# Kernel optimization log

Hardware: AMD Instinct MI355X
Metric: run time of the kernel (lower is better)

## Reference

```python
import jax, jax.numpy as jnp
import numpy as np

HEADS = 8
HEAD_DIM = 32
FOLD = 2
PROP = 2


def l2norm(t):
    n = jnp.linalg.norm(t, axis=-1, keepdims=True)
    return t / jnp.maximum(n, 1e-12)


def conv1x1(x, w, b):
    # x: [B,C,W,H], w: [O,C]
    return jnp.einsum('bchw,oc->bohw', x, w) + b[None, :, None, None]


def avg_pool_to(x, ow, oh):
    b, c, w, h = x.shape
    return x.reshape(b, c, ow, w // ow, oh, h // oh).mean(axis=(3, 5))


def max_pool_to(x, ow, oh):
    b, c, w, h = x.shape
    return x.reshape(b, c, ow, w // ow, oh, h // oh).max(axis=(3, 5))


def centers_offset(x, w1, b1, w2, b2):
    # Mlp_new_offset: avg-pool to (H//4,W//4), channel MLP, max-pool to (2,2)
    b, c, H, W = x.shape
    y = avg_pool_to(x, H // 4, W // 4).transpose(0, 2, 3, 1)  # [b,h4,w4,c]
    y = jax.nn.gelu(y @ w1.T + b1, approximate=False) @ w2.T + b2
    return max_pool_to(y.transpose(0, 3, 1, 2), PROP, PROP)


def fold(t, f):
    b, c, W, H = t.shape
    w, h = W // f, H // f
    return t.reshape(b, c, f, w, f, h).transpose(0, 2, 4, 1, 3, 5).reshape(b * f * f, c, w, h)


def unfold(t, f):
    bf, c, w, h = t.shape
    b = bf // (f * f)
    return t.reshape(b, f, f, c, w, h).transpose(0, 3, 1, 4, 2, 5).reshape(b, c, f * w, f * h)


def setup_inputs() -> dict:
    key = jax.random.key(0)
    ks = jax.random.split(key, 12)
    B, DIM, W, H = 16, 256, 64, 64
    HD = HEADS * HEAD_DIM
    hid = int(HEAD_DIM * 1.66)  # 53
    r = lambda k, s: 0.02 * jax.random.normal(k, s, dtype=jnp.float32)
    return dict(
        x=jax.random.normal(ks[0], (B, DIM, W, H), dtype=jnp.float32),
        gap_scaler=1e-5 * jnp.ones((1, DIM, 1, 1), jnp.float32),
        w_fc1=r(ks[1], (HD, DIM)), b_fc1=r(ks[2], (HD,)),
        w_fcv=r(ks[3], (HD, DIM)), b_fcv=r(ks[4], (HD,)),
        w_fc2=r(ks[5], (DIM, HD)), b_fc2=r(ks[6], (DIM,)),
        sim_alpha=jnp.ones((1,), jnp.float32),
        sim_beta=jnp.zeros((1,), jnp.float32),
        off_w1=r(ks[7], (hid, HEAD_DIM)), off_b1=r(ks[8], (hid,)),
        off_w2=r(ks[9], (HEAD_DIM, hid)), off_b2=r(ks[10], (HEAD_DIM,)),
    )


def reference(x, gap_scaler, w_fc1, b_fc1, w_fcv, b_fcv, w_fc2, b_fc2,
              sim_alpha, sim_beta, off_w1, off_b1, off_w2, off_b2):
    B = x.shape[0]
    x = x + gap_scaler * x.mean(axis=(2, 3), keepdims=True)
    value = conv1x1(x, w_fcv, b_fcv)
    x = conv1x1(x, w_fc1, b_fc1)
    _, _, W, H = x.shape
    Bh = B * HEADS
    x = x.reshape(Bh, HEAD_DIM, W, H)
    value = value.reshape(Bh, HEAD_DIM, W, H)
    x = fold(x, FOLD)
    value = fold(value, FOLD)
    b, c, w, h = x.shape
    N, M = w * h, PROP * PROP
    centers = avg_pool_to(x, PROP, PROP) + centers_offset(x, off_w1, off_b1, off_w2, off_b2)
    value_centers = (avg_pool_to(value, PROP, PROP)
                     + centers_offset(value, off_w1, off_b1, off_w2, off_b2)
                     ).reshape(b, c, M).transpose(0, 2, 1)  # [b,M,c]
    cn = l2norm(centers.reshape(b, c, M).transpose(0, 2, 1))  # [b,M,c]
    xn = l2norm(x.reshape(b, c, N).transpose(0, 2, 1))        # [b,N,c]
    sim = jax.nn.sigmoid(sim_beta + sim_alpha * jnp.einsum('bmc,bnc->bmn', cn, xn))
    # top-1 assignment per token (scatter-built mask in torch)
    idx = jnp.argmax(sim, axis=1)  # [b,N]
    mask = (jnp.arange(M)[None, :, None] == idx[:, None, :]).astype(sim.dtype)
    sim = sim * mask
    value2 = value.reshape(b, c, N).transpose(0, 2, 1)  # [b,N,c]
    # combine: masked weighted sum of tokens into clusters (fused einsum,
    # same math as (value2[:,None]*sim[...,None]).sum(2))
    out = (jnp.einsum('bmn,bnc->bmc', sim, value2) + value_centers) / (mask.sum(-1, keepdims=True) + 1.0)
    # dispatch: broadcast cluster features back to tokens
    out = jnp.einsum('bmc,bmn->bnc', out, sim)
    out = out.transpose(0, 2, 1).reshape(b, c, w, h)
    out = unfold(out, FOLD).reshape(B, HEADS * HEAD_DIM, W, H)
    return conv1x1(out, w_fc2, b_fc2)
```

## Files before the change

### kernel.cpp

```cpp
#include <hip/hip_runtime.h>
#include <hip/hip_bf16.h>
#include <math.h>

#define HID 53

typedef __bf16 bf16x8 __attribute__((ext_vector_type(8)));
typedef float f32x4 __attribute__((ext_vector_type(4)));

__device__ __forceinline__ unsigned f2u(float f) { return __builtin_bit_cast(unsigned, f); }
__device__ __forceinline__ float u2f(unsigned u) { return __builtin_bit_cast(float, u); }
__device__ __forceinline__ bf16x8 ld8(const ushort* p) {
    return __builtin_bit_cast(bf16x8, *(const uint4*)p);
}
__device__ __forceinline__ unsigned rnb(float f) {
    unsigned u = f2u(f);
    return (u + 0x7FFFu + ((u >> 16) & 1u)) >> 16;
}
__device__ __forceinline__ void split3rn(float f, unsigned& h, unsigned& m, unsigned& l) {
    h = rnb(f);
    float r1 = f - u2f(h << 16);
    m = rnb(r1);
    float r2 = r1 - u2f(m << 16);
    l = rnb(r2);
}

__device__ __forceinline__ ushort f2bf(float f) {
    return __builtin_bit_cast(ushort, (__bf16)f);
}
__device__ __forceinline__ float bfbits2f(ushort h) { return u2f((unsigned)h << 16); }
__device__ __forceinline__ void split3c(float f, ushort& h, ushort& m, ushort& l) {
    h = f2bf(f);
    float r1 = f - bfbits2f(h);
    m = f2bf(r1);
    float r2 = r1 - bfbits2f(m);
    l = f2bf(r2);
}

__global__ __launch_bounds__(256) void mean_kernel(
    const float* __restrict__ x, const float* __restrict__ gap,
    float* __restrict__ gmu)
{
    const int bc = blockIdx.x;
    const float* p = x + (size_t)bc * 4096;
    float s = 0.f;
    for (int i = threadIdx.x * 4; i < 4096; i += 256 * 4) {
        float4 v = *(const float4*)(p + i);
        s += v.x + v.y + v.z + v.w;
    }
    s += __shfl_xor(s, 1);
    s += __shfl_xor(s, 2);
    s += __shfl_xor(s, 4);
    s += __shfl_xor(s, 8);
    s += __shfl_xor(s, 16);
    s += __shfl_xor(s, 32);
    __shared__ float ls[4];
    if ((threadIdx.x & 63) == 0) ls[threadIdx.x >> 6] = s;
    __syncthreads();
    if (threadIdx.x == 0) {
        float t = ls[0] + ls[1] + ls[2] + ls[3];
        gmu[bc] = gap[bc & 255] * (t * (1.f / 4096.f));
    }
}

__global__ __launch_bounds__(256, 2) void gemm_xq6_kernel(
    const float* __restrict__ X, const float* __restrict__ gmu,
    const float* __restrict__ W,
    const float* __restrict__ bias_g,
    float* __restrict__ dst)
{
    __shared__ __align__(16) ushort Ahi[128 * 40];
    __shared__ __align__(16) ushort Amd[128 * 40];
    __shared__ __align__(16) ushort Alo[128 * 40];
    __shared__ __align__(16) ushort Bhi[128 * 40];
    __shared__ __align__(16) ushort Bmd[128 * 40];
    __shared__ __align__(16) ushort Blo[128 * 40];

    const int tid  = threadIdx.x;
    const int Nblk = blockIdx.x, Mblk = blockIdx.y, b = blockIdx.z;
    const int lane = tid & 63, wav = tid >> 6;
    const int wm = wav >> 1, wn = wav & 1;
    const int lr = lane & 15, q = lane >> 4;

    f32x4 accM[4][4], accS[4][4];
#pragma unroll
    for (int i = 0; i < 4; ++i)
#pragma unroll
        for (int j = 0; j < 4; ++j) {
            accM[i][j] = (f32x4){0.f, 0.f, 0.f, 0.f};
            accS[i][j] = (f32x4){0.f, 0.f, 0.f, 0.f};
        }

    const bool isB = (tid < 128);
    float4 regs[8];
    float gval0 = 0.f, gval1 = 0.f;
    const float* srcB = X;
    const float* wrow = W;
    int kp = 0, q8 = 0, arow = 0;
    if (isB) {
        kp = tid >> 3; q8 = tid & 7;
        srcB = X + ((size_t)b << 20) + (size_t)(2 * kp) * 4096 + Nblk * 128 + q8 * 4;
    } else {
        arow = tid - 128;
        int o = Mblk * 128 + arow;
        wrow = W + (size_t)o * 256;
    }

    auto LOADR = [&](int ks) {
        const int k0 = ks * 32;
        if (isB) {
            const float* p = srcB + (size_t)k0 * 4096;
#pragma unroll
            for (int i = 0; i < 4; ++i) {
                regs[i]     = *(const float4*)(p + i * 32);
                regs[i + 4] = *(const float4*)(p + 4096 + i * 32);
            }
            gval0 = gmu[b * 256 + k0 + 2 * kp];
            gval1 = gmu[b * 256 + k0 + 2 * kp + 1];
        } else {
            const float* p = wrow + k0;
#pragma unroll
            for (int i = 0; i < 8; ++i) regs[i] = *(const float4*)(p + i * 4);
        }
    };

    auto WRITE = [&]() {
        if (isB) {
#pragma unroll
            for (int i = 0; i < 4; ++i) {
                float4 r0 = regs[i], r1 = regs[i + 4];
                r0.x += gval0; r0.y += gval0; r0.z += gval0; r0.w += gval0;
                r1.x += gval1; r1.y += gval1; r1.z += gval1; r1.w += gval1;
                const float* p0 = &r0.x;
                const float* p1 = &r1.x;
#pragma unroll
                for (int e = 0; e < 4; ++e) {
                    ushort h0, m0, l0, h1, m1, l1;
                    split3c(p0[e], h0, m0, l0);
                    split3c(p1[e], h1, m1, l1);
                    int n = q8 * 4 + i * 32 + e;
                    ((unsigned*)Bhi)[n * 20 + kp] = (unsigned)h0 | ((unsigned)h1 << 16);
                    ((unsigned*)Bmd)[n * 20 + kp] = (unsigned)m0 | ((unsigned)m1 << 16);
                    ((unsigned*)Blo)[n * 20 + kp] = (unsigned)l0 | ((unsigned)l1 << 16);
                }
            }
        } else {
#pragma unroll
            for (int i = 0; i < 8; ++i) {
                float4 r = regs[i];
                ushort h0, m0, l0, h1, m1, l1, h2, m2, l2, h3, m3, l3;
                split3c(r.x, h0, m0, l0);
                split3c(r.y, h1, m1, l1);
                split3c(r.z, h2, m2, l2);
                split3c(r.w, h3, m3, l3);
                uint2 h = {(unsigned)h0 | ((unsigned)h1 << 16),
                           (unsigned)h2 | ((unsigned)h3 << 16)};
                uint2 m = {(unsigned)m0 | ((unsigned)m1 << 16),
                           (unsigned)m2 | ((unsigned)m3 << 16)};
                uint2 l = {(unsigned)l0 | ((unsigned)l1 << 16),
                           (unsigned)l2 | ((unsigned)l3 << 16)};
                *(uint2*)&Ahi[arow * 40 + i * 4] = h;
                *(uint2*)&Amd[arow * 40 + i * 4] = m;
                *(uint2*)&Alo[arow * 40 + i * 4] = l;
            }
        }
    };

    LOADR(0);
    for (int ks = 0; ks < 8; ++ks) {
        WRITE();
        __syncthreads();
        if (ks < 7) LOADR(ks + 1);

        bf16x8 ah[4], ad[4];
#pragma unroll
        for (int mt = 0; mt < 4; ++mt) {
            int row = wm * 64 + mt * 16 + lr;
            ah[mt] = ld8(&Ahi[row * 40 + q * 8]);
            ad[mt] = ld8(&Amd[row * 40 + q * 8]);
        }
#pragma unroll
        for (int nt = 0; nt < 4; ++nt) {
            int row = wn * 64 + nt * 16 + lr;
            bf16x8 bh = ld8(&Bhi[row * 40 + q * 8]);
            bf16x8 bd = ld8(&Bmd[row * 40 + q * 8]);
            bf16x8 bl = ld8(&Blo[row * 40 + q * 8]);
#pragma unroll
            for (int mt = 0; mt < 4; ++mt) {
                accS[mt][nt] = __builtin_amdgcn_mfma_f32_16x16x32_bf16(ah[mt], bd, accS[mt][nt], 0, 0, 0);
                accS[mt][nt] = __builtin_amdgcn_mfma_f32_16x16x32_bf16(ad[mt], bh, accS[mt][nt], 0, 0, 0);
                accS[mt][nt] = __builtin_amdgcn_mfma_f32_16x16x32_bf16(ad[mt], bd, accS[mt][nt], 0, 0, 0);
                accS[mt][nt] = __builtin_amdgcn_mfma_f32_16x16x32_bf16(ah[mt], bl, accS[mt][nt], 0, 0, 0);
                accM[mt][nt] = __builtin_amdgcn_mfma_f32_16x16x32_bf16(ah[mt], bh, accM[mt][nt], 0, 0, 0);
            }
        }
        bf16x8 al[4];
#pragma unroll
        for (int mt = 0; mt < 4; ++mt) {
            int row = wm * 64 + mt * 16 + lr;
            al[mt] = ld8(&Alo[row * 40 + q * 8]);
        }
#pragma unroll
        for (int nt = 0; nt < 4; ++nt) {
            int row = wn * 64 + nt * 16 + lr;
            bf16x8 bh2 = ld8(&Bhi[row * 40 + q * 8]);
#pragma unroll
            for (int mt = 0; mt < 4; ++mt)
                accS[mt][nt] = __builtin_amdgcn_mfma_f32_16x16x32_bf16(al[mt], bh2, accS[mt][nt], 0, 0, 0);
        }
        __syncthreads();
    }

    const size_t bbase = (size_t)b << 20;
    const int tb = Nblk * 128 + wn * 64 + lr;
    int offN[4];
#pragma unroll
    for (int nt = 0; nt < 4; ++nt) {
        int t = tb + nt * 16;
        offN[nt] = ((t >> 11) & 1) * 65536 + ((t >> 5) & 1) * 32768
                 + ((t >> 6) & 31) * 32 + (t & 31);
    }
#pragma unroll
    for (int mt = 0; mt < 4; ++mt) {
#pragma unroll
        for (int r = 0; r < 4; ++r) {
            int oc = Mblk * 128 + wm * 64 + mt * 16 + q * 4 + r;
            float bias = bias_g[oc];
            size_t offM = (size_t)(oc >> 5) * 131072 + (size_t)(oc & 31) * 1024;
#pragma unroll
            for (int nt = 0; nt < 4; ++nt)
                dst[bbase + offM + offN[nt]] = accM[mt][nt][r] + accS[mt][nt][r] + bias;
        }
    }
}

__global__ __launch_bounds__(256, 2) void gemm_val_kernel(
    const float* __restrict__ X, const float* __restrict__ gmu,
    const float* __restrict__ W,
    const float* __restrict__ bias_g,
    float* __restrict__ dst)
{
    __shared__ __align__(16) ushort Ahi[128 * 40];
    __shared__ __align__(16) ushort Amd[128 * 40];
    __shared__ __align__(16) ushort Bhi[128 * 40];
    __shared__ __align__(16) ushort Bmd[128 * 40];

    const int tid  = threadIdx.x;
    const int Nblk = blockIdx.x, Mblk = blockIdx.y, b = blockIdx.z;
    const int lane = tid & 63, wav = tid >> 6;
    const int wm = wav >> 1, wn = wav & 1;
    const int lr = lane & 15, q = lane >> 4;

    f32x4 acc[4][4];
#pragma unroll
    for (int i = 0; i < 4; ++i)
#pragma unroll
        for (int j = 0; j < 4; ++j) acc[i][j] = (f32x4){0.f, 0.f, 0.f, 0.f};

    const bool isB = (tid < 128);
    float4 regs[8];
    float gval0 = 0.f, gval1 = 0.f;
    const float* srcB = X;
    const float* wrow = W;
    int kp = 0, q8 = 0, arow = 0;
    if (isB) {
        kp = tid >> 3; q8 = tid & 7;
        srcB = X + ((size_t)b << 20) + (size_t)(2 * kp) * 4096 + Nblk * 128 + q8 * 4;
    } else {
        arow = tid - 128;
        int o = Mblk * 128 + arow;
        wrow = W + (size_t)o * 256;
    }

    auto LOADR = [&](int ks) {
        const int k0 = ks * 32;
        if (isB) {
            const float* p = srcB + (size_t)k0 * 4096;
#pragma unroll
            for (int i = 0; i < 4; ++i) {
                regs[i]     = *(const float4*)(p + i * 32);
                regs[i + 4] = *(const float4*)(p + 4096 + i * 32);
            }
            gval0 = gmu[b * 256 + k0 + 2 * kp];
            gval1 = gmu[b * 256 + k0 + 2 * kp + 1];
        } else {
            const float* p = wrow + k0;
#pragma unroll
            for (int i = 0; i < 8; ++i) regs[i] = *(const float4*)(p + i * 4);
        }
    };

    auto WRITE = [&]() {
        if (isB) {
#pragma unroll
            for (int i = 0; i < 4; ++i) {
                float4 r0 = regs[i], r1 = regs[i + 4];
                r0.x += gval0; r0.y += gval0; r0.z += gval0; r0.w += gval0;
                r1.x += gval1; r1.y += gval1; r1.z += gval1; r1.w += gval1;
                const float* p0 = &r0.x;
                const float* p1 = &r1.x;
#pragma unroll
                for (int e = 0; e < 4; ++e) {
                    unsigned h0, m0, l0, h1, m1, l1;
                    split3rn(p0[e], h0, m0, l0);
                    split3rn(p1[e], h1, m1, l1);
                    int n = q8 * 4 + i * 32 + e;
                    ((unsigned*)Bhi)[n * 20 + kp] = h0 | (h1 << 16);
                    ((unsigned*)Bmd)[n * 20 + kp] = m0 | (m1 << 16);
                }
            }
        } else {
#pragma unroll
            for (int i = 0; i < 8; ++i) {
                float4 r = regs[i];
                unsigned h0, m0, l0, h1, m1, l1, h2, m2, l2, h3, m3, l3;
                split3rn(r.x, h0, m0, l0);
                split3rn(r.y, h1, m1, l1);
                split3rn(r.z, h2, m2, l2);
                split3rn(r.w, h3, m3, l3);
                uint2 h = {h0 | (h1 << 16), h2 | (h3 << 16)};
                uint2 m = {m0 | (m1 << 16), m2 | (m3 << 16)};
                *(uint2*)&Ahi[arow * 40 + i * 4] = h;
                *(uint2*)&Amd[arow * 40 + i * 4] = m;
            }
        }
    };

    LOADR(0);
    for (int ks = 0; ks < 8; ++ks) {
        WRITE();
        __syncthreads();
        if (ks < 7) LOADR(ks + 1);
        bf16x8 ah[4], ad[4];
#pragma unroll
        for (int mt = 0; mt < 4; ++mt) {
            int row = wm * 64 + mt * 16 + lr;
            ah[mt] = ld8(&Ahi[row * 40 + q * 8]);
            ad[mt] = ld8(&Amd[row * 40 + q * 8]);
        }
#pragma unroll
        for (int nt = 0; nt < 4; ++nt) {
            int row = wn * 64 + nt * 16 + lr;
            bf16x8 bh = ld8(&Bhi[row * 40 + q * 8]);
            bf16x8 bd = ld8(&Bmd[row * 40 + q * 8]);
#pragma unroll
            for (int mt = 0; mt < 4; ++mt) {
                acc[mt][nt] = __builtin_amdgcn_mfma_f32_16x16x32_bf16(ah[mt], bd, acc[mt][nt], 0, 0, 0);
                acc[mt][nt] = __builtin_amdgcn_mfma_f32_16x16x32_bf16(ad[mt], bh, acc[mt][nt], 0, 0, 0);
                acc[mt][nt] = __builtin_amdgcn_mfma_f32_16x16x32_bf16(ah[mt], bh, acc[mt][nt], 0, 0, 0);
            }
        }
        __syncthreads();
    }

    const size_t bbase = (size_t)b << 20;
    const int tb = Nblk * 128 + wn * 64 + lr;
    int offN[4];
#pragma unroll
    for (int nt = 0; nt < 4; ++nt) {
        int t = tb + nt * 16;
        offN[nt] = ((t >> 11) & 1) * 65536 + ((t >> 5) & 1) * 32768
                 + ((t >> 6) & 31) * 32 + (t & 31);
    }
#pragma unroll
    for (int mt = 0; mt < 4; ++mt) {
#pragma unroll
        for (int r = 0; r < 4; ++r) {
            int oc = Mblk * 128 + wm * 64 + mt * 16 + q * 4 + r;
            float bias = bias_g[oc];
            size_t offM = (size_t)(oc >> 5) * 131072 + (size_t)(oc & 31) * 1024;
#pragma unroll
            for (int nt = 0; nt < 4; ++nt)
                dst[bbase + offM + offN[nt]] = acc[mt][nt][r] + bias;
        }
    }
}

__global__ __launch_bounds__(256) void pool_kernel(
    const float* __restrict__ xqb, const float* __restrict__ valb,
    float* __restrict__ pzg)
{
    const int bp   = blockIdx.x;
    const int srci = blockIdx.y;
    const int ch   = blockIdx.z;
    const float* src = (srci ? valb : xqb) + (size_t)bp * 32768 + ch * 16384;
    const int t  = threadIdx.x;
    const int cl = t >> 4;
    const int gh = (t >> 1) & 7;
    const int s  = t & 1;

    const float* p0 = src + cl * 1024 + gh * 4;
    float acc[4];
#pragma unroll
    for (int j = 0; j < 4; ++j) {
        const float* p = p0 + (s * 4 + j) * 128;
        float a = 0.f;
#pragma unroll
        for (int i = 0; i < 4; ++i) {
            float4 v = *(const float4*)(p + i * 32);
            a += (v.x + v.y) + (v.z + v.w);
        }
        acc[j] = a * 0.0625f;
    }
    float* dstb = pzg + (size_t)(srci * 512 + bp) * 2048 + (ch * 16 + cl);
#pragma unroll
    for (int j = 0; j < 4; ++j) {
        int g = (s * 4 + j) * 8 + gh;
        dstb[g * 32] = acc[j];
    }
}

__global__ __launch_bounds__(256) void centers_mlp_kernel(
    const float* __restrict__ pzg,
    const float* __restrict__ w1g, const float* __restrict__ b1g,
    const float* __restrict__ w2g, const float* __restrict__ b2g,
    float* __restrict__ cenbuf)
{
    const int bp   = blockIdx.x;
    const int srci = blockIdx.y;
    const int t    = threadIdx.x;

    __shared__ float pzs[2048];
    __shared__ float ybuf[64 * HID];
    __shared__ float w1t[32 * HID];
    __shared__ float w2s[32 * HID];
    __shared__ float b1s[56];
    __shared__ float b2s[32];
    __shared__ float avg2[128];

    const float* psrc = pzg + (size_t)(srci * 512 + bp) * 2048;
    for (int i = t; i < 2048; i += 256) pzs[i] = psrc[i];
    for (int i = t; i < 32 * HID; i += 256) {
        int h = i >> 5, c = i & 31;
        w1t[c * HID + h] = w1g[i];
        w2s[i] = w2g[i];
    }
    if (t < HID) b1s[t] = b1g[t];
    if (t < 32) b2s[t] = b2g[t];
    __syncthreads();

    if (t < 128) {
        int qq = t >> 5, c = t & 31, qw = qq >> 1, qh = qq & 1;
        float s = 0.f;
        for (int a = 0; a < 4; ++a)
            for (int e = 0; e < 4; ++e)
                s += pzs[((qw * 4 + a) * 8 + (qh * 4 + e)) * 32 + c];
        avg2[t] = s * 0.0625f;
    }
    for (int tt = t; tt < 64 * HID; tt += 256) {
        int g = tt / HID, h = tt - g * HID;
        float a = b1s[h];
        for (int c = 0; c < 32; ++c)
            a = fmaf(pzs[g * 32 + c], w1t[c * HID + h], a);
        ybuf[g * HID + h] = 0.5f * a * (1.f + erff(a * 0.70710678118654752f));
    }
    __syncthreads();

    for (int tt = t; tt < 2048; tt += 256) {
        int g = tt >> 5, c = tt & 31;
        float a = b2s[c];
        for (int h = 0; h < HID; ++h)
            a = fmaf(ybuf[g * HID + h], w2s[c * HID + h], a);
        pzs[tt] = a;
    }
    __syncthreads();

    if (t < 128) {
        int qq = t >> 5, c = t & 31, qw = qq >> 1, qh = qq & 1;
        float m = -1e30f;
        for (int a = 0; a < 4; ++a)
            for (int e = 0; e < 4; ++e)
                m = fmaxf(m, pzs[((qw * 4 + a) * 8 + qh * 4 + e) * 32 + c]);
        cenbuf[srci * 65536 + bp * 128 + t] = avg2[t] + m;
    }
}

__global__ __launch_bounds__(1024) void assign_kernel(
    const float* __restrict__ xqb, const float* __restrict__ valb,
    const float* __restrict__ cenbuf,
    const float* __restrict__ alphap, const float* __restrict__ betap,
    float* __restrict__ wbpk, float* __restrict__ outcg)
{
    const int bp = blockIdx.x;
    const int n  = threadIdx.x;
    const int lane = n & 63;

    __shared__ float cen0s[128], cen1s[128];
    __shared__ float wbuf[1024];
    __shared__ int   bbuf[1024];
    __shared__ float csum[32][4];
    __shared__ float ccnt[4];

    if (n < 128) cen0s[n] = cenbuf[bp * 128 + n];
    else if (n < 256) cen1s[n - 128] = cenbuf[65536 + bp * 128 + (n - 128)];
    if (n < 4) ccnt[n] = 0.f;
    __syncthreads();

    float rn[4];
#pragma unroll
    for (int m = 0; m < 4; ++m) {
        float ssn = 0.f;
        for (int c = 0; c < 32; ++c) { float tt = cen0s[m * 32 + c]; ssn += tt * tt; }
        rn[m] = 1.f / fmaxf(sqrtf(ssn), 1e-12f);
    }

    const float* px = xqb + (size_t)bp * 32768 + n;
    float ss = 0.f, d0 = 0.f, d1 = 0.f, d2 = 0.f, d3 = 0.f;
#pragma unroll
    for (int c = 0; c < 32; ++c) {
        float v = px[(size_t)c << 10];
        ss += v * v;
        d0 += cen0s[0 * 32 + c] * v;
        d1 += cen0s[1 * 32 + c] * v;
        d2 += cen0s[2 * 32 + c] * v;
        d3 += cen0s[3 * 32 + c] * v;
    }
    const float rx = 1.f / fmaxf(sqrtf(ss), 1e-12f);
    const float alpha = alphap[0], beta = betap[0];
    float dm[4] = {d0, d1, d2, d3};
    float best = -1.f;
    int bidx = 0;
#pragma unroll
    for (int m = 0; m < 4; ++m) {
        float t = beta + alpha * (dm[m] * rn[m] * rx);
        float s = 1.f / (1.f + expf(-t));
        if (m == 0 || s > best) { best = s; bidx = m; }
    }
    wbuf[n] = best;
    bbuf[n] = bidx;
    wbpk[(size_t)bp * 1024 + n] = u2f((f2u(best) & ~3u) | (unsigned)bidx);

#pragma unroll
    for (int m = 0; m < 4; ++m) {
        unsigned long long bl = __ballot(bidx == m);
        if (lane == 0) atomicAdd(&ccnt[m], (float)__popcll(bl));
    }
    __syncthreads();

    {
        const int c = n >> 5, l = n & 31;
        const float* pv = valb + (size_t)bp * 32768 + c * 1024 + l;
        float a0 = 0.f, a1 = 0.f, a2 = 0.f, a3 = 0.f;
#pragma unroll
        for (int i = 0; i < 32; ++i) {
            float v = pv[i * 32];
            int t = i * 32 + l;
            float p = wbuf[t] * v;
            int m = bbuf[t];
            a0 += (m == 0) ? p : 0.f;
            a1 += (m == 1) ? p : 0.f;
            a2 += (m == 2) ? p : 0.f;
            a3 += (m == 3) ? p : 0.f;
        }
#pragma unroll
        for (int off = 1; off < 32; off <<= 1) {
            a0 += __shfl_xor(a0, off);
            a1 += __shfl_xor(a1, off);
            a2 += __shfl_xor(a2, off);
            a3 += __shfl_xor(a3, off);
        }
        if (l == 0) {
            csum[c][0] = a0; csum[c][1] = a1; csum[c][2] = a2; csum[c][3] = a3;
        }
    }
    __syncthreads();
    if (n < 128)
        outcg[(size_t)bp * 128 + n] =
            (csum[n & 31][n >> 5] + cen1s[n]) / (ccnt[n >> 5] + 1.f);
}

__global__ __launch_bounds__(256) void pmat_kernel(
    const float* __restrict__ outcg, const float* __restrict__ w2,
    float* __restrict__ P)
{
    const int bp = blockIdx.x;
    const int o  = threadIdx.x;
    __shared__ float oc[128];
    if (o < 128) oc[o] = outcg[(size_t)bp * 128 + o];
    __syncthreads();
    const int head = (bp >> 2) & 7;
    const float* wrow = w2 + (size_t)o * 256 + head * 32;
    float a0 = 0.f, a1 = 0.f, a2 = 0.f, a3 = 0.f;
#pragma unroll
    for (int c = 0; c < 32; ++c) {
        float wv = wrow[c];
        a0 = fmaf(wv, oc[c], a0);
        a1 = fmaf(wv, oc[32 + c], a1);
        a2 = fmaf(wv, oc[64 + c], a2);
        a3 = fmaf(wv, oc[96 + c], a3);
    }
    float* pb = P + (size_t)bp * 1024;
    pb[0 * 256 + o] = a0;
    pb[1 * 256 + o] = a1;
    pb[2 * 256 + o] = a2;
    pb[3 * 256 + o] = a3;
}

__global__ __launch_bounds__(1024) void fc2_dispatch_kernel(
    const float* __restrict__ P, const float* __restrict__ wbpk,
    const float* __restrict__ b2, float* __restrict__ out)
{
    const int ogrp = blockIdx.x, quad = blockIdx.y, b = blockIdx.z;
    const int n = threadIdx.x;
    const int wl = n >> 5, hl = n & 31;

    __shared__ float Pl[8][4][68];
    __shared__ float b2s[64];

    for (int i = n; i < 2048; i += 1024) {
        int h = i >> 8, rm = i & 255;
        int m = rm >> 6, j = rm & 63;
        int bp = b * 32 + h * 4 + quad;
        Pl[h][m][j] = P[(size_t)bp * 1024 + m * 256 + ogrp * 64 + j];
    }
    if (n < 64) b2s[n] = b2[ogrp * 64 + n];
    __syncthreads();

    float bst[8];
    int   mm[8];
#pragma unroll
    for (int h = 0; h < 8; ++h) {
        int bp = b * 32 + h * 4 + quad;
        unsigned u = f2u(wbpk[(size_t)bp * 1024 + n]);
        mm[h]  = (int)(u & 3u);
        bst[h] = u2f(u & ~3u);
    }

    const int fi = quad >> 1, fj = quad & 1;
    float* obp = out + (size_t)b * 1048576 + (size_t)ogrp * 64 * 4096
               + (size_t)(fi * 32 + wl) * 64 + (fj * 32 + hl);
#pragma unroll 4
    for (int j = 0; j < 64; ++j) {
        float s = b2s[j];
#pragma unroll
        for (int h = 0; h < 8; ++h)
            s = fmaf(bst[h], Pl[h][mm[h]][j], s);
        obp[(size_t)j * 4096] = s;
    }
}

extern "C" void kernel_launch(void* const* d_in, const int* in_sizes, int n_in,
                              void* d_out, int out_size, void* d_ws, size_t ws_size,
                              hipStream_t stream) {
    const float* x     = (const float*)d_in[0];
    const float* gap   = (const float*)d_in[1];
    const float* wq    = (const float*)d_in[2];
    const float* bq    = (const float*)d_in[3];
    const float* wv    = (const float*)d_in[4];
    const float* bv    = (const float*)d_in[5];
    const float* w2    = (const float*)d_in[6];
    const float* b2    = (const float*)d_in[7];
    const float* alpha = (const float*)d_in[8];
    const float* beta  = (const float*)d_in[9];
    const float* ow1   = (const float*)d_in[10];
    const float* ob1   = (const float*)d_in[11];
    const float* ow2   = (const float*)d_in[12];
    const float* ob2   = (const float*)d_in[13];

    float* out  = (float*)d_out;
    float* gmu  = (float*)d_ws;
    float* valb = gmu + 4096;
    float* cenb = valb + (size_t)16777216;
    float* wbpk = cenb + 131072;
    float* outc = wbpk + 524288;
    float* pmat = outc + 65536;
    float* pzg  = pmat + 524288;
    float* xqb  = out;

    mean_kernel<<<4096, 256, 0, stream>>>(x, gap, gmu);
    gemm_xq6_kernel<<<dim3(32, 2, 16), 256, 0, stream>>>(x, gmu, wq, bq, xqb);
    gemm_val_kernel<<<dim3(32, 2, 16), 256, 0, stream>>>(x, gmu, wv, bv, valb);
    pool_kernel<<<dim3(512, 2, 2), 256, 0, stream>>>(xqb, valb, pzg);
    centers_mlp_kernel<<<dim3(512, 2), 256, 0, stream>>>(
        pzg, ow1, ob1, ow2, ob2, cenb);
    assign_kernel<<<512, 1024, 0, stream>>>(
        xqb, valb, cenb, alpha, beta, wbpk, outc);
    pmat_kernel<<<512, 256, 0, stream>>>(outc, w2, pmat);
    fc2_dispatch_kernel<<<dim3(4, 4, 16), 1024, 0, stream>>>(
        pmat, wbpk, b2, out);
}
```

Before: 228.4 us.

## Pre-split weights to bf16 planes once and load A fragments from global memory

```diff
diff --git a/kernel.cpp b/kernel.cpp
--- a/kernel.cpp
+++ b/kernel.cpp
@@ -11,17 +11,6 @@
 __device__ __forceinline__ float u2f(unsigned u) { return __builtin_bit_cast(float, u); }
 __device__ __forceinline__ bf16x8 ld8(const ushort* p) {
     return __builtin_bit_cast(bf16x8, *(const uint4*)p);
-}
-__device__ __forceinline__ unsigned rnb(float f) {
-    unsigned u = f2u(f);
-    return (u + 0x7FFFu + ((u >> 16) & 1u)) >> 16;
-}
-__device__ __forceinline__ void split3rn(float f, unsigned& h, unsigned& m, unsigned& l) {
-    h = rnb(f);
-    float r1 = f - u2f(h << 16);
-    m = rnb(r1);
-    float r2 = r1 - u2f(m << 16);
-    l = rnb(r2);
 }
 
 __device__ __forceinline__ ushort f2bf(float f) {
@@ -34,6 +23,19 @@
     m = f2bf(r1);
     float r2 = r1 - bfbits2f(m);
     l = f2bf(r2);
+}
+
+__global__ __launch_bounds__(256) void wsplit_kernel(
+    const float* __restrict__ wq, const float* __restrict__ wv,
+    ushort* __restrict__ qhi, ushort* __restrict__ qmd, ushort* __restrict__ qlo,
+    ushort* __restrict__ vhi, ushort* __restrict__ vmd)
+{
+    const int id = blockIdx.x * 256 + threadIdx.x;
+    ushort h, m, l;
+    split3c(wq[id], h, m, l);
+    qhi[id] = h; qmd[id] = m; qlo[id] = l;
+    split3c(wv[id], h, m, l);
+    vhi[id] = h; vmd[id] = m;
 }
 
 __global__ __launch_bounds__(256) void mean_kernel(
@@ -64,16 +66,14 @@
 
 __global__ __launch_bounds__(256, 2) void gemm_xq6_kernel(
     const float* __restrict__ X, const float* __restrict__ gmu,
-    const float* __restrict__ W,
+    const ushort* __restrict__ Whi, const ushort* __restrict__ Wmd,
+    const ushort* __restrict__ Wlo,
     const float* __restrict__ bias_g,
     float* __restrict__ dst)
 {
-    __shared__ __align__(16) ushort Ahi[128 * 40];
-    __shared__ __align__(16) ushort Amd[128 * 40];
-    __shared__ __align__(16) ushort Alo[128 * 40];
-    __shared__ __align__(16) ushort Bhi[128 * 40];
-    __shared__ __align__(16) ushort Bmd[128 * 40];
-    __shared__ __align__(16) ushort Blo[128 * 40];
+    __shared__ __align__(16) ushort Bhi[128 * 36];
+    __shared__ __align__(16) ushort Bmd[128 * 36];
+    __shared__ __align__(16) ushort Blo[128 * 36];
 
     const int tid  = threadIdx.x;
     const int Nblk = blockIdx.x, Mblk = blockIdx.y, b = blockIdx.z;
@@ -90,77 +90,50 @@
             accS[i][j] = (f32x4){0.f, 0.f, 0.f, 0.f};
         }
 
-    const bool isB = (tid < 128);
-    float4 regs[8];
+    const int kp = tid & 15;
+    const int q8 = (tid >> 4) & 7;
+    const int ih = tid >> 7;
+    const float* srcB = X + ((size_t)b << 20) + (size_t)(2 * kp) * 4096
+                      + Nblk * 128 + q8 * 4;
+    const float* gmub = gmu + b * 256;
+
+    const size_t wbase = (size_t)(Mblk * 128 + wm * 64) * 256;
+    const ushort* pwh = Whi + wbase;
+    const ushort* pwd = Wmd + wbase;
+    const ushort* pwl = Wlo + wbase;
+
+    float4 regs[4];
     float gval0 = 0.f, gval1 = 0.f;
-    const float* srcB = X;
-    const float* wrow = W;
-    int kp = 0, q8 = 0, arow = 0;
-    if (isB) {
-        kp = tid >> 3; q8 = tid & 7;
-        srcB = X + ((size_t)b << 20) + (size_t)(2 * kp) * 4096 + Nblk * 128 + q8 * 4;
-    } else {
-        arow = tid - 128;
-        int o = Mblk * 128 + arow;
-        wrow = W + (size_t)o * 256;
-    }
 
     auto LOADR = [&](int ks) {
         const int k0 = ks * 32;
-        if (isB) {
-            const float* p = srcB + (size_t)k0 * 4096;
-#pragma unroll
-            for (int i = 0; i < 4; ++i) {
-                regs[i]     = *(const float4*)(p + i * 32);
-                regs[i + 4] = *(const float4*)(p + 4096 + i * 32);
-            }
-            gval0 = gmu[b * 256 + k0 + 2 * kp];
-            gval1 = gmu[b * 256 + k0 + 2 * kp + 1];
-        } else {
-            const float* p = wrow + k0;
-#pragma unroll
-            for (int i = 0; i < 8; ++i) regs[i] = *(const float4*)(p + i * 4);
-        }
+        const float* p = srcB + (size_t)k0 * 4096;
+        regs[0] = *(const float4*)(p + (ih * 2 + 0) * 32);
+        regs[1] = *(const float4*)(p + 4096 + (ih * 2 + 0) * 32);
+        regs[2] = *(const float4*)(p + (ih * 2 + 1) * 32);
+        regs[3] = *(const float4*)(p + 4096 + (ih * 2 + 1) * 32);
+        gval0 = gmub[k0 + 2 * kp];
+        gval1 = gmub[k0 + 2 * kp + 1];
     };
 
     auto WRITE = [&]() {
-        if (isB) {
-#pragma unroll
-            for (int i = 0; i < 4; ++i) {
-                float4 r0 = regs[i], r1 = regs[i + 4];
-                r0.x += gval0; r0.y += gval0; r0.z += gval0; r0.w += gval0;
-                r1.x += gval1; r1.y += gval1; r1.z += gval1; r1.w += gval1;
-                const float* p0 = &r0.x;
-                const float* p1 = &r1.x;
-#pragma unroll
-                for (int e = 0; e < 4; ++e) {
-                    ushort h0, m0, l0, h1, m1, l1;
-                    split3c(p0[e], h0, m0, l0);
-                    split3c(p1[e], h1, m1, l1);
-                    int n = q8 * 4 + i * 32 + e;
-                    ((unsigned*)Bhi)[n * 20 + kp] = (unsigned)h0 | ((unsigned)h1 << 16);
-                    ((unsigned*)Bmd)[n * 20 + kp] = (unsigned)m0 | ((unsigned)m1 << 16);
-                    ((unsigned*)Blo)[n * 20 + kp] = (unsigned)l0 | ((unsigned)l1 << 16);
-                }
-            }
-        } else {
-#pragma unroll
-            for (int i = 0; i < 8; ++i) {
-                float4 r = regs[i];
-                ushort h0, m0, l0, h1, m1, l1, h2, m2, l2, h3, m3, l3;
-                split3c(r.x, h0, m0, l0);
-                split3c(r.y, h1, m1, l1);
-                split3c(r.z, h2, m2, l2);
-                split3c(r.w, h3, m3, l3);
-                uint2 h = {(unsigned)h0 | ((unsigned)h1 << 16),
-                           (unsigned)h2 | ((unsigned)h3 << 16)};
-                uint2 m = {(unsigned)m0 | ((unsigned)m1 << 16),
-                           (unsigned)m2 | ((unsigned)m3 << 16)};
-                uint2 l = {(unsigned)l0 | ((unsigned)l1 << 16),
-                           (unsigned)l2 | ((unsigned)l3 << 16)};
-                *(uint2*)&Ahi[arow * 40 + i * 4] = h;
-                *(uint2*)&Amd[arow * 40 + i * 4] = m;
-                *(uint2*)&Alo[arow * 40 + i * 4] = l;
+#pragma unroll
+        for (int ii = 0; ii < 2; ++ii) {
+            const int i = ih * 2 + ii;
+            float4 r0 = regs[ii * 2], r1 = regs[ii * 2 + 1];
+            r0.x += gval0; r0.y += gval0; r0.z += gval0; r0.w += gval0;
+            r1.x += gval1; r1.y += gval1; r1.z += gval1; r1.w += gval1;
+            const float* p0 = &r0.x;
+            const float* p1 = &r1.x;
+#pragma unroll
+            for (int e = 0; e < 4; ++e) {
+                ushort h0, m0, l0, h1, m1, l1;
+                split3c(p0[e], h0, m0, l0);
+                split3c(p1[e], h1, m1, l1);
+                const int n = q8 * 4 + i * 32 + e;
+                ((unsigned*)Bhi)[n * 18 + kp] = (unsigned)h0 | ((unsigned)h1 << 16);
+                ((unsigned*)Bmd)[n * 18 + kp] = (unsigned)m0 | ((unsigned)m1 << 16);
+                ((unsigned*)Blo)[n * 18 + kp] = (unsigned)l0 | ((unsigned)l1 << 16);
             }
         }
     };
@@ -171,19 +144,20 @@
         __syncthreads();
         if (ks < 7) LOADR(ks + 1);
 
+        const int koff = ks * 32 + q * 8;
         bf16x8 ah[4], ad[4];
 #pragma unroll
         for (int mt = 0; mt < 4; ++mt) {
-            int row = wm * 64 + mt * 16 + lr;
-            ah[mt] = ld8(&Ahi[row * 40 + q * 8]);
-            ad[mt] = ld8(&Amd[row * 40 + q * 8]);
+            const size_t off = (size_t)(mt * 16 + lr) * 256 + koff;
+            ah[mt] = ld8(pwh + off);
+            ad[mt] = ld8(pwd + off);
         }
 #pragma unroll
         for (int nt = 0; nt < 4; ++nt) {
-            int row = wn * 64 + nt * 16 + lr;
-            bf16x8 bh = ld8(&Bhi[row * 40 + q * 8]);
-            bf16x8 bd = ld8(&Bmd[row * 40 + q * 8]);
-            bf16x8 bl = ld8(&Blo[row * 40 + q * 8]);
+            const int row = wn * 64 + nt * 16 + lr;
+            bf16x8 bh = ld8(&Bhi[row * 36 + q * 8]);
+            bf16x8 bd = ld8(&Bmd[row * 36 + q * 8]);
+            bf16x8 bl = ld8(&Blo[row * 36 + q * 8]);
 #pragma unroll
             for (int mt = 0; mt < 4; ++mt) {
                 accS[mt][nt] = __builtin_amdgcn_mfma_f32_16x16x32_bf16(ah[mt], bd, accS[mt][nt], 0, 0, 0);
@@ -196,13 +170,13 @@
         bf16x8 al[4];
 #pragma unroll
         for (int mt = 0; mt < 4; ++mt) {
-            int row = wm * 64 + mt * 16 + lr;
-            al[mt] = ld8(&Alo[row * 40 + q * 8]);
+            const size_t off = (size_t)(mt * 16 + lr) * 256 + koff;
+            al[mt] = ld8(pwl + off);
         }
 #pragma unroll
         for (int nt = 0; nt < 4; ++nt) {
-            int row = wn * 64 + nt * 16 + lr;
-            bf16x8 bh2 = ld8(&Bhi[row * 40 + q * 8]);
+            const int row = wn * 64 + nt * 16 + lr;
+            bf16x8 bh2 = ld8(&Bhi[row * 36 + q * 8]);
 #pragma unroll
             for (int mt = 0; mt < 4; ++mt)
                 accS[mt][nt] = __builtin_amdgcn_mfma_f32_16x16x32_bf16(al[mt], bh2, accS[mt][nt], 0, 0, 0);
@@ -233,16 +207,14 @@
     }
 }
 
-__global__ __launch_bounds__(256, 2) void gemm_val_kernel(
+__global__ __launch_bounds__(256, 4) void gemm_val_kernel(
     const float* __restrict__ X, const float* __restrict__ gmu,
-    const float* __restrict__ W,
+    const ushort* __restrict__ Whi, const ushort* __restrict__ Wmd,
     const float* __restrict__ bias_g,
     float* __restrict__ dst)
 {
-    __shared__ __align__(16) ushort Ahi[128 * 40];
-    __shared__ __align__(16) ushort Amd[128 * 40];
-    __shared__ __align__(16) ushort Bhi[128 * 40];
-    __shared__ __align__(16) ushort Bmd[128 * 40];
+    __shared__ __align__(16) ushort Bhi[128 * 36];
+    __shared__ __align__(16) ushort Bmd[128 * 36];
 
     const int tid  = threadIdx.x;
     const int Nblk = blockIdx.x, Mblk = blockIdx.y, b = blockIdx.z;
@@ -256,71 +228,48 @@
 #pragma unroll
         for (int j = 0; j < 4; ++j) acc[i][j] = (f32x4){0.f, 0.f, 0.f, 0.f};
 
-    const bool isB = (tid < 128);
-    float4 regs[8];
+    const int kp = tid & 15;
+    const int q8 = (tid >> 4) & 7;
+    const int ih = tid >> 7;
+    const float* srcB = X + ((size_t)b << 20) + (size_t)(2 * kp) * 4096
+                      + Nblk * 128 + q8 * 4;
+    const float* gmub = gmu + b * 256;
+
+    const size_t wbase = (size_t)(Mblk * 128 + wm * 64) * 256;
+    const ushort* pwh = Whi + wbase;
+    const ushort* pwd = Wmd + wbase;
+
+    float4 regs[4];
     float gval0 = 0.f, gval1 = 0.f;
-    const float* srcB = X;
-    const float* wrow = W;
-    int kp = 0, q8 = 0, arow = 0;
-    if (isB) {
-        kp = tid >> 3; q8 = tid & 7;
-        srcB = X + ((size_t)b << 20) + (size_t)(2 * kp) * 4096 + Nblk * 128 + q8 * 4;
-    } else {
-        arow = tid - 128;
-        int o = Mblk * 128 + arow;
-        wrow = W + (size_t)o * 256;
-    }
 
     auto LOADR = [&](int ks) {
         const int k0 = ks * 32;
-        if (isB) {
-            const float* p = srcB + (size_t)k0 * 4096;
-#pragma unroll
-            for (int i = 0; i < 4; ++i) {
-                regs[i]     = *(const float4*)(p + i * 32);
-                regs[i + 4] = *(const float4*)(p + 4096 + i * 32);
-            }
-            gval0 = gmu[b * 256 + k0 + 2 * kp];
-            gval1 = gmu[b * 256 + k0 + 2 * kp + 1];
-        } else {
-            const float* p = wrow + k0;
-#pragma unroll
-            for (int i = 0; i < 8; ++i) regs[i] = *(const float4*)(p + i * 4);
-        }
+        const float* p = srcB + (size_t)k0 * 4096;
+        regs[0] = *(const float4*)(p + (ih * 2 + 0) * 32);
+        regs[1] = *(const float4*)(p + 4096 + (ih * 2 + 0) * 32);
+        regs[2] = *(const float4*)(p + (ih * 2 + 1) * 32);
+        regs[3] = *(const float4*)(p + 4096 + (ih * 2 + 1) * 32);
+        gval0 = gmub[k0 + 2 * kp];
+        gval1 = gmub[k0 + 2 * kp + 1];
     };
 
     auto WRITE = [&]() {
-        if (isB) {
-#pragma unroll
-            for (int i = 0; i < 4; ++i) {
-                float4 r0 = regs[i], r1 = regs[i + 4];
-                r0.x += gval0; r0.y += gval0; r0.z += gval0; r0.w += gval0;
-                r1.x += gval1; r1.y += gval1; r1.z += gval1; r1.w += gval1;
-                const float* p0 = &r0.x;
-                const float* p1 = &r1.x;
-#pragma unroll
-                for (int e = 0; e < 4; ++e) {
-                    unsigned h0, m0, l0, h1, m1, l1;
-                    split3rn(p0[e], h0, m0, l0);
-                    split3rn(p1[e], h1, m1, l1);
-                    int n = q8 * 4 + i * 32 + e;
-                    ((unsigned*)Bhi)[n * 20 + kp] = h0 | (h1 << 16);
-                    ((unsigned*)Bmd)[n * 20 + kp] = m0 | (m1 << 16);
-                }
-            }
-        } else {
-#pragma unroll
-            for (int i = 0; i < 8; ++i) {
-                float4 r = regs[i];
-                unsigned h0, m0, l0, h1, m1, l1, h2, m2, l2, h3, m3, l3;
-                split3rn(r.x, h0, m0, l0);
-                split3rn(r.y, h1, m1, l1);
-                split3rn(r.z, h2, m2, l2);
-                split3rn(r.w, h3, m3, l3);
-                uint2 h = {h0 | (h1 << 16), h2 | (h3 << 16)};
-                uint2 m = {m0 | (m1 << 16), m2 | (m3 << 16)};
-                *(uint2*)&Ahi[arow * 40 + i * 4] = h;
-                *(uint2*)&Amd[arow * 40 + i * 4] = m;
+#pragma unroll
+        for (int ii = 0; ii < 2; ++ii) {
+            const int i = ih * 2 + ii;
+            float4 r0 = regs[ii * 2], r1 = regs[ii * 2 + 1];
+            r0.x += gval0; r0.y += gval0; r0.z += gval0; r0.w += gval0;
+            r1.x += gval1; r1.y += gval1; r1.z += gval1; r1.w += gval1;
+            const float* p0 = &r0.x;
+            const float* p1 = &r1.x;
+#pragma unroll
+            for (int e = 0; e < 4; ++e) {
+                ushort h0, m0, l0, h1, m1, l1;
+                split3c(p0[e], h0, m0, l0);
+                split3c(p1[e], h1, m1, l1);
+                const int n = q8 * 4 + i * 32 + e;
+                ((unsigned*)Bhi)[n * 18 + kp] = (unsigned)h0 | ((unsigned)h1 << 16);
+                ((unsigned*)Bmd)[n * 18 + kp] = (unsigned)m0 | ((unsigned)m1 << 16);
             }
         }
     };
@@ -330,18 +279,20 @@
         WRITE();
         __syncthreads();
         if (ks < 7) LOADR(ks + 1);
+
+        const int koff = ks * 32 + q * 8;
         bf16x8 ah[4], ad[4];
 #pragma unroll
         for (int mt = 0; mt < 4; ++mt) {
-            int row = wm * 64 + mt * 16 + lr;
-            ah[mt] = ld8(&Ahi[row * 40 + q * 8]);
-            ad[mt] = ld8(&Amd[row * 40 + q * 8]);
+            const size_t off = (size_t)(mt * 16 + lr) * 256 + koff;
+            ah[mt] = ld8(pwh + off);
+            ad[mt] = ld8(pwd + off);
         }
 #pragma unroll
         for (int nt = 0; nt < 4; ++nt) {
-            int row = wn * 64 + nt * 16 + lr;
-            bf16x8 bh = ld8(&Bhi[row * 40 + q * 8]);
-            bf16x8 bd = ld8(&Bmd[row * 40 + q * 8]);
+            const int row = wn * 64 + nt * 16 + lr;
+            bf16x8 bh = ld8(&Bhi[row * 36 + q * 8]);
+            bf16x8 bd = ld8(&Bmd[row * 36 + q * 8]);
 #pragma unroll
             for (int mt = 0; mt < 4; ++mt) {
                 acc[mt][nt] = __builtin_amdgcn_mfma_f32_16x16x32_bf16(ah[mt], bd, acc[mt][nt], 0, 0, 0);
@@ -664,11 +615,19 @@
     float* outc = wbpk + 524288;
     float* pmat = outc + 65536;
     float* pzg  = pmat + 524288;
+    ushort* wqh = (ushort*)(pzg + 2097152);
+    ushort* wqm = wqh + 65536;
+    ushort* wql = wqm + 65536;
+    ushort* wvh = wql + 65536;
+    ushort* wvm = wvh + 65536;
     float* xqb  = out;
 
+    wsplit_kernel<<<256, 256, 0, stream>>>(wq, wv, wqh, wqm, wql, wvh, wvm);
     mean_kernel<<<4096, 256, 0, stream>>>(x, gap, gmu);
-    gemm_xq6_kernel<<<dim3(32, 2, 16), 256, 0, stream>>>(x, gmu, wq, bq, xqb);
-    gemm_val_kernel<<<dim3(32, 2, 16), 256, 0, stream>>>(x, gmu, wv, bv, valb);
+    gemm_xq6_kernel<<<dim3(32, 2, 16), 256, 0, stream>>>(
+        x, gmu, wqh, wqm, wql, bq, xqb);
+    gemm_val_kernel<<<dim3(32, 2, 16), 256, 0, stream>>>(
+        x, gmu, wvh, wvm, bv, valb);
     pool_kernel<<<dim3(512, 2, 2), 256, 0, stream>>>(xqb, valb, pzg);
     centers_mlp_kernel<<<dim3(512, 2), 256, 0, stream>>>(
         pzg, ow1, ob1, ow2, ob2, cenb);
```

Result: slower. 260.7 us (+14.1%).
